# Kernel tuning notes

Measured on AMD Instinct MI355X. Metric: run time of the kernel, lower is better.

Reference implementation:

```python
import jax, jax.numpy as jnp
import numpy as np

N_NODES = 50000
N_EDGES = 800000
NEG_SLOPE = 0.2


def _gat_conv(h, src, dst, W, al, ar, b, res, act):
    """DGL-style GATConv. h:[N,Fin], W:[Fin,H*D], al/ar:[H,D], b:[H*D].
    res: None | [N,H,D] residual value. Returns [N,H,D]."""
    N = h.shape[0]
    H, D = al.shape
    ft = (h @ W).reshape(N, H, D)                       # projected features
    el = jnp.einsum('nhd,hd->nh', ft, al)               # [N,H]
    er = jnp.einsum('nhd,hd->nh', ft, ar)               # [N,H]
    e = jax.nn.leaky_relu(el[src] + er[dst], NEG_SLOPE) # [E,H] edge logits
    # edge softmax over incoming edges of each dst node
    emax = jax.ops.segment_max(e, dst, num_segments=N)  # [N,H]
    emax = jnp.where(jnp.isfinite(emax), emax, 0.0)     # guard empty segments
    ex = jnp.exp(e - emax[dst])                         # [E,H]
    denom = jax.ops.segment_sum(ex, dst, num_segments=N)
    a = ex / denom[dst]                                 # [E,H] attention
    rst = jax.ops.segment_sum(ft[src] * a[..., None], dst, num_segments=N)  # [N,H,D]
    if res is not None:
        rst = rst + res
    rst = rst + b.reshape(1, H, D)
    if act is not None:
        rst = act(rst)
    return rst


def setup_inputs() -> dict:
    key = jax.random.key(0)
    ks = jax.random.split(key, 16)
    s = 0.1
    return {
        'x': jax.random.normal(ks[0], (N_NODES, 128), jnp.float32),
        'edge_src': jax.random.randint(ks[1], (N_EDGES,), 0, N_NODES, jnp.int32),
        'edge_dst': jax.random.randint(ks[2], (N_EDGES,), 0, N_NODES, jnp.int32),
        'W0': jax.random.normal(ks[3], (128, 128), jnp.float32) * s,
        'al0': jax.random.normal(ks[4], (2, 64), jnp.float32) * s,
        'ar0': jax.random.normal(ks[5], (2, 64), jnp.float32) * s,
        'b0': jnp.zeros((128,), jnp.float32),
        'W1': jax.random.normal(ks[6], (128, 128), jnp.float32) * s,
        'al1': jax.random.normal(ks[7], (2, 64), jnp.float32) * s,
        'ar1': jax.random.normal(ks[8], (2, 64), jnp.float32) * s,
        'b1': jnp.zeros((128,), jnp.float32),
        'W2': jax.random.normal(ks[9], (128, 194), jnp.float32) * s,
        'al2': jax.random.normal(ks[10], (2, 97), jnp.float32) * s,
        'ar2': jax.random.normal(ks[11], (2, 97), jnp.float32) * s,
        'b2': jnp.zeros((194,), jnp.float32),
        'res_W2': jax.random.normal(ks[12], (128, 194), jnp.float32) * s,
    }


def reference(x, edge_src, edge_dst, W0, al0, ar0, b0, W1, al1, ar1, b1,
              W2, al2, ar2, b2, res_W2):
    N = x.shape[0]
    elu = jax.nn.elu
    # layer 0: no residual, ELU
    h = _gat_conv(x, edge_src, edge_dst, W0, al0, ar0, b0, None, elu)
    h = h.reshape(N, -1)                                # flatten(1) -> [N,128]
    # layer 1: identity residual (in == heads*out), ELU
    res1 = h.reshape(N, 2, 64)
    h = _gat_conv(h, edge_src, edge_dst, W1, al1, ar1, b1, res1, elu)
    h = h.reshape(N, -1)
    # output layer: linear residual, no activation, mean over heads
    res2 = (h @ res_W2).reshape(N, 2, 97)
    logits = _gat_conv(h, edge_src, edge_dst, W2, al2, ar2, b2, res2, None)
    logits = logits.mean(axis=1)                        # [N, 97]
    # original slices off the last node of each graph (single batched graph)
    return logits[: N - 1]
```

## Files before the change

kernel.cpp:

```cpp
#include <hip/hip_runtime.h>
#include <math.h>

#define NNODES 50000
#define NEDGES 800000
#define NPAD   50048

typedef unsigned int uint;
typedef unsigned short u16;
typedef __bf16 bf16x8 __attribute__((ext_vector_type(8)));
typedef float f32x4 __attribute__((ext_vector_type(4)));

__device__ __forceinline__ float lrelu(float x){ return x > 0.f ? x : 0.2f*x; }
__device__ __forceinline__ float elu_f(float x){ return x > 0.f ? x : expm1f(x); }
__device__ __forceinline__ u16 f2bf(float f){
    uint u = __float_as_uint(f);
    return (u16)((u + 0x7fffu + ((u >> 16) & 1u)) >> 16);
}
__device__ __forceinline__ float bf2f(u16 h){ return __uint_as_float(((uint)h) << 16); }
__device__ __forceinline__ float blo(uint u){ return __uint_as_float(u << 16); }
__device__ __forceinline__ float bhi(uint u){ return __uint_as_float(u & 0xffff0000u); }

#define R0 (NPAD*32)
#define R1 (R0 + 256*128)
#define R2 (R1 + 128*384)
#define R3 (R2 + 256)
#define R4 (R3 + 128)
__global__ void prep_all(const float* __restrict__ x,
                         const float* __restrict__ W0, const float* __restrict__ W1,
                         const float* __restrict__ W2, const float* __restrict__ Wr,
                         const float* __restrict__ al2, const float* __restrict__ ar2,
                         const float* __restrict__ b2,
                         u16* __restrict__ Xb, u16* __restrict__ H1b,
                         u16* __restrict__ B01, u16* __restrict__ Bf,
                         float* __restrict__ alp2, float* __restrict__ arp2,
                         float* __restrict__ cb, int N)
{
    int idx = blockIdx.x * blockDim.x + threadIdx.x;
    if (idx < R0) {
        int n = idx >> 5;
        ushort4 hv = make_ushort4(0,0,0,0);
        if (n < N) {
            float4 v = ((const float4*)x)[idx];
            hv.x = f2bf(v.x); hv.y = f2bf(v.y); hv.z = f2bf(v.z); hv.w = f2bf(v.w);
        } else {
            ((ushort4*)H1b)[idx] = make_ushort4(0,0,0,0);
        }
        ((ushort4*)Xb)[idx] = hv;
    } else if (idx < R1) {
        int j = idx - R0, gcol = j >> 7, k = j & 127;
        float v = (gcol < 128) ? W0[k*128 + gcol] : W1[k*128 + (gcol - 128)];
        B01[j] = f2bf(v);
    } else if (idx < R2) {
        int j = idx - R1, c = j / 384, k = j - c*384;
        float v = 0.f;
        if (c < 97) {
            if (k < 128)      v = W2[k*194 + c];
            else if (k < 256) v = W2[(k-128)*194 + 97 + c];
            else              v = Wr[(k-256)*194 + c] + Wr[(k-256)*194 + 97 + c];
        }
        Bf[c*384 + k] = f2bf(v);
    } else if (idx < R3) {
        int t = idx - R2, k = t & 127, h = t >> 7;
        float sl = 0.f, sr = 0.f;
        for (int d = 0; d < 97; d++) {
            float w = W2[k*194 + h*97 + d];
            sl += w * al2[h*97 + d];
            sr += w * ar2[h*97 + d];
        }
        alp2[h*128 + k] = sl;
        arp2[h*128 + k] = sr;
    } else if (idx < R4) {
        int c = idx - R3;
        if (c < 97) cb[c] = 0.5f * (b2[c] + b2[97 + c]);
    }
}

__global__ __launch_bounds__(256, 4)
void gemm_l01(const u16* __restrict__ Ab, const u16* __restrict__ Bh, u16* __restrict__ obf,
              const float* __restrict__ alv, const float* __restrict__ arv,
              float* __restrict__ el, float* __restrict__ er, int N)
{
    __shared__ u16 sB[128 * 136];
    const int bm = blockIdx.x * 64;
    const int tid = threadIdx.x, wid = tid >> 6, lane = tid & 63;
    const int lr = lane & 15, q = lane >> 4, lk8 = q << 3;

    bf16x8 aH[4];
    {
        size_t abase = (size_t)(bm + wid*16 + lr) * 128 + lk8;
        #pragma unroll
        for (int kt = 0; kt < 4; kt++)
            aH[kt] = *(const bf16x8*)(Ab + abase + kt*32);
    }
    {
        const int c = tid >> 1, seg = (tid & 1) * 64;
        const u16* g = Bh + (size_t)c * 128 + seg;
        u16* s = sB + c * 136 + seg;
        #pragma unroll
        for (int j = 0; j < 8; j++)
            *(uint4*)(s + j*8) = *(const uint4*)(g + j*8);
    }
    __syncthreads();

    f32x4 acc[8];
    #pragma unroll
    for (int i = 0; i < 8; i++) acc[i] = (f32x4){0.f,0.f,0.f,0.f};

    #pragma unroll
    for (int kt = 0; kt < 4; kt++)
        #pragma unroll
        for (int fs = 0; fs < 8; fs++) {
            bf16x8 b = *(const bf16x8*)(sB + (fs*16 + lr)*136 + kt*32 + lk8);
            acc[fs] = __builtin_amdgcn_mfma_f32_16x16x32_bf16(aH[kt], b, acc[fs], 0, 0, 0);
        }

    float el0[4] = {0,0,0,0}, el1[4] = {0,0,0,0}, er0[4] = {0,0,0,0}, er1[4] = {0,0,0,0};
    #pragma unroll
    for (int fs = 0; fs < 8; fs++) {
        const int col = fs*16 + lr;
        const float av = alv[col], gv = arv[col];
        #pragma unroll
        for (int v = 0; v < 4; v++) {
            float f = acc[fs][v];
            int row = bm + wid*16 + q*4 + v;
            if (row < N) obf[(size_t)row * 128 + col] = f2bf(f);
            if (fs < 4) { el0[v] += f * av; er0[v] += f * gv; }
            else        { el1[v] += f * av; er1[v] += f * gv; }
        }
    }
    #pragma unroll
    for (int off = 1; off < 16; off <<= 1) {
        #pragma unroll
        for (int v = 0; v < 4; v++) {
            el0[v] += __shfl_xor(el0[v], off);
            el1[v] += __shfl_xor(el1[v], off);
            er0[v] += __shfl_xor(er0[v], off);
            er1[v] += __shfl_xor(er1[v], off);
        }
    }
    if (lr == 0) {
        #pragma unroll
        for (int v = 0; v < 4; v++) {
            int row = bm + wid*16 + q*4 + v;
            if (row < N) {
                *(float2*)(el + 2*(size_t)row) = make_float2(el0[v], el1[v]);
                *(float2*)(er + 2*(size_t)row) = make_float2(er0[v], er1[v]);
            }
        }
    }
}

__global__ __launch_bounds__(256, 3)
void gemm_final(const u16* __restrict__ agg01, const u16* __restrict__ h2b,
                const u16* __restrict__ Bf, const float* __restrict__ cb,
                float* __restrict__ out, int N)
{
    __shared__ u16 sB[64 * 392];
    const int bid = blockIdx.x;
    const int x = (bid >> 4) * 8 + (bid & 7);
    const int ct = (bid >> 3) & 1;
    if (x >= NPAD / 64) return;
    const int bm = x * 64;
    const int tid = threadIdx.x, wid = tid >> 6, lane = tid & 63;
    const int lr = lane & 15, q = lane >> 4, lk8 = q << 3;

    bf16x8 aF[12];
    {
        const int row = bm + wid*16 + lr;
        const u16* pa = agg01 + (size_t)row * 256;
        #pragma unroll
        for (int kt = 0; kt < 8; kt++)
            aF[kt] = *(const bf16x8*)(pa + kt*32 + lk8);
        const u16* ph = h2b + (size_t)row * 128;
        #pragma unroll
        for (int kt = 0; kt < 4; kt++)
            aF[8 + kt] = *(const bf16x8*)(ph + kt*32 + lk8);
    }
    {
        const int c = tid >> 2, seg = (tid & 3) * 96;
        const u16* g = Bf + (size_t)(ct*64 + c) * 384 + seg;
        u16* s = sB + c * 392 + seg;
        #pragma unroll
        for (int j = 0; j < 12; j++)
            *(uint4*)(s + j*8) = *(const uint4*)(g + j*8);
    }
    __syncthreads();

    f32x4 acc[4];
    #pragma unroll
    for (int i = 0; i < 4; i++) acc[i] = (f32x4){0.f,0.f,0.f,0.f};

    #pragma unroll
    for (int kt = 0; kt < 12; kt++)
        #pragma unroll
        for (int fs = 0; fs < 4; fs++) {
            bf16x8 b = *(const bf16x8*)(sB + (fs*16 + lr)*392 + kt*32 + lk8);
            acc[fs] = __builtin_amdgcn_mfma_f32_16x16x32_bf16(aF[kt], b, acc[fs], 0, 0, 0);
        }

    #pragma unroll
    for (int fs = 0; fs < 4; fs++) {
        const int col = ct*64 + fs*16 + lr;
        if (col >= 97) continue;
        const float cbc = cb[col];
        #pragma unroll
        for (int v = 0; v < 4; v++) {
            int row = bm + wid*16 + q*4 + v;
            if (row < N - 1) out[(size_t)row * 97 + col] = 0.5f * acc[fs][v] + cbc;
        }
    }
}

__global__ void hist_kernel(const int* __restrict__ dst, int* __restrict__ counts, int E)
{
    int i = blockIdx.x * blockDim.x + threadIdx.x;
    if (i < E) atomicAdd(&counts[dst[i]], 1);
}

__global__ __launch_bounds__(1024)
void scan_dl(int* __restrict__ cnt_cur, int* __restrict__ row_start,
             int* __restrict__ flags, int* __restrict__ prefixes, int n)
{
    __shared__ int wsum[16];
    __shared__ int sExc;
    const int tid = threadIdx.x, lane = tid & 63, wv = tid >> 6;
    const int i0 = blockIdx.x * 4096 + tid * 4;
    int c[4], v[4];
    #pragma unroll
    for (int j = 0; j < 4; j++) { int i = i0 + j; c[j] = (i < n) ? cnt_cur[i] : 0; }
    v[0] = c[0]; v[1] = v[0] + c[1]; v[2] = v[1] + c[2]; v[3] = v[2] + c[3];
    int t = v[3];
    #pragma unroll
    for (int off = 1; off < 64; off <<= 1) {
        int u = __shfl_up(t, off);
        if (lane >= off) t += u;
    }
    int texcl = t - v[3];
    if (lane == 63) wsum[wv] = t;
    __syncthreads();
    if (tid == 0) {
        int tot = 0;
        #pragma unroll
        for (int w = 0; w < 16; w++) tot += wsum[w];
        int exc = 0;
        if (blockIdx.x > 0) {
            while (atomicAdd(&flags[blockIdx.x - 1], 0) == 0) __builtin_amdgcn_s_sleep(2);
            exc = atomicAdd(&prefixes[blockIdx.x - 1], 0);
        } else {
            row_start[0] = 0;
        }
        atomicExch(&prefixes[blockIdx.x], exc + tot);
        __threadfence();
        atomicExch(&flags[blockIdx.x], 1);
        sExc = exc;
    }
    __syncthreads();
    int woff = sExc + texcl;
    for (int w = 0; w < 16; w++) if (w < wv) woff += wsum[w];
    #pragma unroll
    for (int j = 0; j < 4; j++) {
        int i = i0 + j;
        if (i < n) {
            int inc = woff + v[j];
            row_start[i + 1] = inc;
            cnt_cur[i] = inc - c[j];
        }
    }
}

__global__ void scatter_kernel(const int* __restrict__ src, const int* __restrict__ dst,
                               int* __restrict__ cursor, int* __restrict__ src_sorted, int E)
{
    int i = blockIdx.x * blockDim.x + threadIdx.x;
    if (i < E) {
        int p = atomicAdd(&cursor[dst[i]], 1);
        src_sorted[p] = src[i];
    }
}

template<int MODE>
__global__ __launch_bounds__(256)
void gat_agg128(const uint* __restrict__ ftb, const float* __restrict__ el,
                const float* __restrict__ er, const int* __restrict__ row_start,
                const int* __restrict__ ssorted, const u16* __restrict__ Rb,
                const float* __restrict__ bias, u16* __restrict__ Hb,
                const float* __restrict__ alp2, const float* __restrict__ arp2,
                float* __restrict__ el2, float* __restrict__ er2)
{
    __shared__ int   s_src[4][64];
    __shared__ float s_w[4][2][64];
    const int wv = threadIdx.x >> 6, lane = threadIdx.x & 63;
    const int n = blockIdx.x * 4 + wv;
    const int beg = row_start[n];
    const int deg = row_start[n+1] - beg;
    const float2 ern = *(const float2*)(er + 2*(size_t)n);
    const int h = lane >> 5;
    float ax = 0.f, ay = 0.f, dp0 = 0.f, dp1 = 0.f;

    for (int cb = 0; cb < deg; cb += 64) {
        const int cnt = min(64, deg - cb);
        float w0 = 0.f, w1 = 0.f; int s = 0;
        if (lane < cnt) {
            s = ssorted[beg + cb + lane];
            float2 e = *(const float2*)(el + 2*(size_t)s);
            w0 = __expf(lrelu(e.x + ern.x));
            w1 = __expf(lrelu(e.y + ern.y));
        }
        dp0 += w0; dp1 += w1;
        s_src[wv][lane] = s; s_w[wv][0][lane] = w0; s_w[wv][1][lane] = w1;
        asm volatile("s_waitcnt lgkmcnt(0)" ::: "memory");
        int t = 0;
        for (; t + 8 <= cnt; t += 8) {
            int4   sa = *(const int4*)&s_src[wv][t];
            int4   sb = *(const int4*)&s_src[wv][t+4];
            float4 wa = *(const float4*)&s_w[wv][h][t];
            float4 wb = *(const float4*)&s_w[wv][h][t+4];
            int   sv[8] = {sa.x,sa.y,sa.z,sa.w,sb.x,sb.y,sb.z,sb.w};
            float wj[8] = {wa.x,wa.y,wa.z,wa.w,wb.x,wb.y,wb.z,wb.w};
            uint U[8];
            #pragma unroll
            for (int j = 0; j < 8; j++) U[j] = ftb[((uint)sv[j] << 6) + lane];
            #pragma unroll
            for (int j = 0; j < 8; j++) { ax += wj[j]*blo(U[j]); ay += wj[j]*bhi(U[j]); }
        }
        for (; t < cnt; t++) {
            int sv = s_src[wv][t];
            float w = s_w[wv][h][t];
            uint u = ftb[((uint)sv << 6) + lane];
            ax += w*blo(u); ay += w*bhi(u);
        }
    }
    #pragma unroll
    for (int off = 32; off; off >>= 1) { dp0 += __shfl_xor(dp0, off); dp1 += __shfl_xor(dp1, off); }
    const float den = (h == 0) ? dp0 : dp1;
    float r0 = (deg > 0) ? ax / den : 0.f;
    float r1 = (deg > 0) ? ay / den : 0.f;
    const int c0 = 2 * lane;
    const size_t ob = (size_t)n*128 + c0;
    const float2 bv = *(const float2*)(bias + c0);
    float v0 = r0 + bv.x, v1 = r1 + bv.y;
    if (MODE == 1) {
        ushort2 rv = *(const ushort2*)&Rb[ob];
        v0 += bf2f(rv.x);
        v1 += bf2f(rv.y);
    }
    v0 = elu_f(v0); v1 = elu_f(v1);
    *(ushort2*)&Hb[ob] = make_ushort2(f2bf(v0), f2bf(v1));

    if constexpr (MODE == 1) {
        float2 a0 = *(const float2*)(alp2 + c0);
        float2 a1 = *(const float2*)(alp2 + 128 + c0);
        float2 g0 = *(const float2*)(arp2 + c0);
        float2 g1 = *(const float2*)(arp2 + 128 + c0);
        float e0 = v0*a0.x + v1*a0.y;
        float e1 = v0*a1.x + v1*a1.y;
        float f0 = v0*g0.x + v1*g0.y;
        float f1 = v0*g1.x + v1*g1.y;
        #pragma unroll
        for (int off = 32; off; off >>= 1) {
            e0 += __shfl_xor(e0, off); e1 += __shfl_xor(e1, off);
            f0 += __shfl_xor(f0, off); f1 += __shfl_xor(f1, off);
        }
        if (lane == 0) {
            *(float2*)(el2 + 2*(size_t)n) = make_float2(e0, e1);
            *(float2*)(er2 + 2*(size_t)n) = make_float2(f0, f1);
        }
    }
}

__global__ __launch_bounds__(256)
void gat_agg_out2(const uint* __restrict__ h2u, const float* __restrict__ el,
                  const float* __restrict__ er, const int* __restrict__ row_start,
                  const int* __restrict__ ssorted, u16* __restrict__ agg01)
{
    __shared__ int   s_src[4][64];
    __shared__ float s_w[4][2][64];
    const int wv = threadIdx.x >> 6, lane = threadIdx.x & 63;
    const int n = blockIdx.x * 4 + wv;
    const int beg = row_start[n];
    const int deg = row_start[n+1] - beg;
    const float2 ern = *(const float2*)(er + 2*(size_t)n);
    float ax0 = 0.f, ay0 = 0.f, ax1 = 0.f, ay1 = 0.f, dp0 = 0.f, dp1 = 0.f;

    for (int cb = 0; cb < deg; cb += 64) {
        const int cnt = min(64, deg - cb);
        float w0 = 0.f, w1 = 0.f; int s = 0;
        if (lane < cnt) {
            s = ssorted[beg + cb + lane];
            float2 e = *(const float2*)(el + 2*(size_t)s);
            w0 = __expf(lrelu(e.x + ern.x));
            w1 = __expf(lrelu(e.y + ern.y));
        }
        dp0 += w0; dp1 += w1;
        s_src[wv][lane] = s; s_w[wv][0][lane] = w0; s_w[wv][1][lane] = w1;
        asm volatile("s_waitcnt lgkmcnt(0)" ::: "memory");
        int t = 0;
        for (; t + 8 <= cnt; t += 8) {
            int4   sa = *(const int4*)&s_src[wv][t];
            int4   sb = *(const int4*)&s_src[wv][t+4];
            float4 p0a = *(const float4*)&s_w[wv][0][t];
            float4 p0b = *(const float4*)&s_w[wv][0][t+4];
            float4 p1a = *(const float4*)&s_w[wv][1][t];
            float4 p1b = *(const float4*)&s_w[wv][1][t+4];
            int   sv[8] = {sa.x,sa.y,sa.z,sa.w,sb.x,sb.y,sb.z,sb.w};
            float f0[8] = {p0a.x,p0a.y,p0a.z,p0a.w,p0b.x,p0b.y,p0b.z,p0b.w};
            float f1[8] = {p1a.x,p1a.y,p1a.z,p1a.w,p1b.x,p1b.y,p1b.z,p1b.w};
            uint U[8];
            #pragma unroll
            for (int j = 0; j < 8; j++) U[j] = h2u[((uint)sv[j] << 6) + lane];
            #pragma unroll
            for (int j = 0; j < 8; j++) {
                float lo = blo(U[j]), hi = bhi(U[j]);
                ax0 += f0[j]*lo; ay0 += f0[j]*hi;
                ax1 += f1[j]*lo; ay1 += f1[j]*hi;
            }
        }
        for (; t < cnt; t++) {
            int sv = s_src[wv][t];
            float f0 = s_w[wv][0][t], f1 = s_w[wv][1][t];
            uint u = h2u[((uint)sv << 6) + lane];
            float lo = blo(u), hi = bhi(u);
            ax0 += f0*lo; ay0 += f0*hi;
            ax1 += f1*lo; ay1 += f1*hi;
        }
    }
    #pragma unroll
    for (int off = 32; off; off >>= 1) { dp0 += __shfl_xor(dp0, off); dp1 += __shfl_xor(dp1, off); }
    const float i0 = (deg > 0) ? 1.f/dp0 : 0.f;
    const float i1 = (deg > 0) ? 1.f/dp1 : 0.f;
    const int c0 = 2 * lane;
    *(ushort2*)&agg01[(size_t)n*256 + c0]       = make_ushort2(f2bf(ax0*i0), f2bf(ay0*i0));
    *(ushort2*)&agg01[(size_t)n*256 + 128 + c0] = make_ushort2(f2bf(ax1*i1), f2bf(ay1*i1));
}

extern "C" void kernel_launch(void* const* d_in, const int* in_sizes, int n_in,
                              void* d_out, int out_size, void* d_ws, size_t ws_size,
                              hipStream_t stream)
{
    const float* x   = (const float*)d_in[0];
    const int*   esrc= (const int*)  d_in[1];
    const int*   edst= (const int*)  d_in[2];
    const float* W0  = (const float*)d_in[3];
    const float* al0 = (const float*)d_in[4];
    const float* ar0 = (const float*)d_in[5];
    const float* b0  = (const float*)d_in[6];
    const float* W1  = (const float*)d_in[7];
    const float* al1 = (const float*)d_in[8];
    const float* ar1 = (const float*)d_in[9];
    const float* b1  = (const float*)d_in[10];
    const float* W2  = (const float*)d_in[11];
    const float* al2 = (const float*)d_in[12];
    const float* ar2 = (const float*)d_in[13];
    const float* b2  = (const float*)d_in[14];
    const float* rW2 = (const float*)d_in[15];
    float* out = (float*)d_out;

    const int N = NNODES, E = NEDGES;
    const int NB = (N + 4095) / 4096;
    float* ws = (float*)d_ws;
    size_t o = 0;
    auto alloc_f = [&](size_t count) { float* p = ws + o; o += (count + 3) & ~(size_t)3; return p; };
    float* el    = alloc_f((size_t)N * 2);
    float* er    = alloc_f((size_t)N * 2);
    float* el2   = alloc_f((size_t)N * 2);
    float* er2   = alloc_f((size_t)N * 2);
    uint*  ftb   = (uint*)alloc_f((size_t)N * 64);
    u16*   agg01 = (u16*)alloc_f((size_t)NPAD * 128);
    u16*   Xb    = (u16*)alloc_f((size_t)NPAD * 64);
    u16*   H1b   = (u16*)alloc_f((size_t)NPAD * 64);
    u16*   B01   = (u16*)alloc_f(256 * 64);
    u16*   Bf    = (u16*)alloc_f(128 * 192);
    float* alp2  = alloc_f(256);
    float* arp2  = alloc_f(256);
    float* cbv   = alloc_f(128);
    int* row_start = (int*)alloc_f(N + 4);
    int* cursor    = (int*)alloc_f(N + 64);
    int* flags     = cursor + N;
    int* prefixes  = cursor + N + 16;
    int* ssorted   = (int*)alloc_f(E);

    hipMemsetAsync(cursor, 0, (N + 64) * sizeof(int), stream);
    hist_kernel<<<(E + 255) / 256, 256, 0, stream>>>(edst, cursor, E);
    scan_dl<<<NB, 1024, 0, stream>>>(cursor, row_start, flags, prefixes, N);
    scatter_kernel<<<(E + 255) / 256, 256, 0, stream>>>(esrc, edst, cursor, ssorted, E);

    prep_all<<<(R4 + 255) / 256, 256, 0, stream>>>(x, W0, W1, W2, rW2, al2, ar2, b2,
                                                   Xb, H1b, B01, Bf, alp2, arp2, cbv, N);

    const int gx = NPAD / 64;
    const int agg_grid = N / 4;

    gemm_l01<<<gx, 256, 0, stream>>>(Xb, B01, (u16*)ftb, al0, ar0, el, er, N);
    gat_agg128<0><<<agg_grid, 256, 0, stream>>>(ftb, el, er, row_start, ssorted,
                                                nullptr, b0, H1b, nullptr, nullptr, nullptr, nullptr);

    gemm_l01<<<gx, 256, 0, stream>>>(H1b, B01 + 128*128, (u16*)ftb, al1, ar1, el, er, N);
    gat_agg128<1><<<agg_grid, 256, 0, stream>>>(ftb, el, er, row_start, ssorted,
                                                H1b, b1, Xb, alp2, arp2, el2, er2);

    gat_agg_out2<<<agg_grid, 256, 0, stream>>>((uint*)Xb, el2, er2, row_start, ssorted, agg01);
    gemm_final<<<((gx + 7) / 8) * 16, 256, 0, stream>>>(agg01, Xb, Bf, cbv, out, N);
}
```

Baseline: 297.0 us.

## Slice CSR histogram and scatter by destination range per block group

Replaces the one-edge-per-thread histogram and scatter kernels with grid-stride versions where each block is assigned one of 8 destination-node slices and only handles edges whose dst falls in that slice. The aim is to localize atomics and scattered writes to a smaller address range per block (better L2/XCD locality on the multi-die GPU). In exchange every edge's dst is read 8 times and src is read in the scatter pass, adding redundant loads and branch divergence.

```diff
diff --git a/kernel.cpp b/kernel.cpp
--- a/kernel.cpp
+++ b/kernel.cpp
@@ -4,6 +4,8 @@
 #define NNODES 50000
 #define NEDGES 800000
 #define NPAD   50048
+#define NSLICE 8
+#define SLICEN (NNODES / NSLICE)
 
 typedef unsigned int uint;
 typedef unsigned short u16;
@@ -211,10 +213,32 @@
     }
 }
 
-__global__ void hist_kernel(const int* __restrict__ dst, int* __restrict__ counts, int E)
-{
-    int i = blockIdx.x * blockDim.x + threadIdx.x;
-    if (i < E) atomicAdd(&counts[dst[i]], 1);
+__global__ __launch_bounds__(256)
+void hist_sliced(const int* __restrict__ dst, int* __restrict__ counts, int E)
+{
+    const int slice = blockIdx.x & (NSLICE - 1);
+    const int lo = slice * SLICEN, hi = lo + SLICEN;
+    const int stride = (gridDim.x >> 3) * blockDim.x;
+    for (int i = (blockIdx.x >> 3) * blockDim.x + threadIdx.x; i < E; i += stride) {
+        int d = dst[i];
+        if (d >= lo && d < hi) atomicAdd(&counts[d], 1);
+    }
+}
+
+__global__ __launch_bounds__(256)
+void scatter_sliced(const int* __restrict__ src, const int* __restrict__ dst,
+                    int* __restrict__ cursor, int* __restrict__ ssorted, int E)
+{
+    const int slice = blockIdx.x & (NSLICE - 1);
+    const int lo = slice * SLICEN, hi = lo + SLICEN;
+    const int stride = (gridDim.x >> 3) * blockDim.x;
+    for (int i = (blockIdx.x >> 3) * blockDim.x + threadIdx.x; i < E; i += stride) {
+        int d = dst[i];
+        if (d >= lo && d < hi) {
+            int p = atomicAdd(&cursor[d], 1);
+            ssorted[p] = src[i];
+        }
+    }
 }
 
 __global__ __launch_bounds__(1024)
@@ -265,16 +289,6 @@
             row_start[i + 1] = inc;
             cnt_cur[i] = inc - c[j];
         }
-    }
-}
-
-__global__ void scatter_kernel(const int* __restrict__ src, const int* __restrict__ dst,
-                               int* __restrict__ cursor, int* __restrict__ src_sorted, int E)
-{
-    int i = blockIdx.x * blockDim.x + threadIdx.x;
-    if (i < E) {
-        int p = atomicAdd(&cursor[dst[i]], 1);
-        src_sorted[p] = src[i];
     }
 }
 
@@ -480,9 +494,9 @@
     int* ssorted   = (int*)alloc_f(E);
 
     hipMemsetAsync(cursor, 0, (N + 64) * sizeof(int), stream);
-    hist_kernel<<<(E + 255) / 256, 256, 0, stream>>>(edst, cursor, E);
+    hist_sliced<<<NSLICE * 256, 256, 0, stream>>>(edst, cursor, E);
     scan_dl<<<NB, 1024, 0, stream>>>(cursor, row_start, flags, prefixes, N);
-    scatter_kernel<<<(E + 255) / 256, 256, 0, stream>>>(esrc, edst, cursor, ssorted, E);
+    scatter_sliced<<<NSLICE * 256, 256, 0, stream>>>(esrc, edst, cursor, ssorted, E);
 
     prep_all<<<(R4 + 255) / 256, 256, 0, stream>>>(x, W0, W1, W2, rW2, al2, ar2, b2,
                                                    Xb, H1b, B01, Bf, alp2, arp2, cbv, N);
```

Result: faster. 281.2 us (-5.3%).
